# Kernel optimization log

Hardware: AMD Instinct MI355X
Metric: run time of the kernel (lower is better)

Reference implementation:

```python
import jax, jax.numpy as jnp
import numpy as np

EPS = 1e-15
BN_EPS = 1e-5
N_NODES = 50000
N_EDGES = 800000
IN_CH = 32
OUT_CH = 32
DIM = 3


def _gmm_params(key, in_ch, out_ch, K):
    k1, k2, k3, k4 = jax.random.split(key, 4)
    g = jax.random.normal(k1, (in_ch, K * out_ch), jnp.float32) * (1.0 / np.sqrt(in_ch))
    mu = jax.random.normal(k2, (K, DIM), jnp.float32)
    sigma = jax.random.uniform(k3, (K, DIM), jnp.float32, 0.5, 1.5)
    root = jax.random.normal(k4, (in_ch, out_ch), jnp.float32) * (1.0 / np.sqrt(in_ch))
    bias = jnp.zeros((out_ch,), jnp.float32)
    return g, mu, sigma, root, bias


def setup_inputs() -> dict:
    key = jax.random.key(0)
    ks = jax.random.split(key, 12)
    x = jax.random.normal(ks[0], (N_NODES, IN_CH), jnp.float32)
    edge_index = jax.random.randint(ks[1], (2, N_EDGES), 0, N_NODES, jnp.int64)
    edge_attr = jax.random.uniform(ks[2], (N_EDGES, DIM), jnp.float32)
    g1, mu1, sig1, root1, b1 = _gmm_params(ks[3], IN_CH, OUT_CH, 5)
    g2, mu2, sig2, root2, b2 = _gmm_params(ks[4], OUT_CH, OUT_CH, 5)
    gs, mus, sigs, roots, bs = _gmm_params(ks[5], IN_CH, OUT_CH, 1)
    ones = jnp.ones((OUT_CH,), jnp.float32)
    zeros = jnp.zeros((OUT_CH,), jnp.float32)
    return dict(x=x, edge_attr=edge_attr,
                g1=g1, mu1=mu1, sig1=sig1, root1=root1, b1=b1, gam1=ones, bet1=zeros,
                g2=g2, mu2=mu2, sig2=sig2, root2=root2, b2=b2, gam2=ones, bet2=zeros,
                gs=gs, mus=mus, sigs=sigs, roots=roots, bs=bs, gams=ones, bets=zeros,
                edge_index=edge_index)


def gmm_conv(x, edge_index, edge_attr, g, mu, sigma, root, bias, num_nodes):
    # PyG GMMConv (separate kernels=False, aggr='mean', root_weight=True)
    src, dst = edge_index[0], edge_index[1]
    K = mu.shape[0]
    out_ch = root.shape[1]
    # Gaussian mixture weights per edge/kernel: [E, K]
    diff = edge_attr[:, None, :] - mu[None, :, :]               # [E, K, D]
    w = jnp.exp(jnp.sum(-0.5 * diff * diff / (EPS + sigma[None] ** 2), axis=-1))
    # Project and gather source features: [E, K, out]
    xj = (x @ g).reshape(-1, K, out_ch)[src] if False else (x[src] @ g).reshape(-1, K, out_ch)
    msg = jnp.einsum('ek,ekc->ec', w, xj)                        # [E, out]
    agg = jax.ops.segment_sum(msg, dst, num_segments=num_nodes)
    cnt = jax.ops.segment_sum(jnp.ones((msg.shape[0],), msg.dtype), dst, num_segments=num_nodes)
    agg = agg / jnp.maximum(cnt, 1.0)[:, None]                   # mean aggregation
    return agg + x @ root + bias


def batch_norm(x, gamma, beta):
    mean = jnp.mean(x, axis=0)
    var = jnp.var(x, axis=0)
    return gamma * (x - mean) * jax.lax.rsqrt(var + BN_EPS) + beta


def reference(x, edge_attr,
              g1, mu1, sig1, root1, b1, gam1, bet1,
              g2, mu2, sig2, root2, b2, gam2, bet2,
              gs, mus, sigs, roots, bs, gams, bets,
              edge_index):
    n = x.shape[0]
    h = jax.nn.elu(batch_norm(gmm_conv(x, edge_index, edge_attr, g1, mu1, sig1, root1, b1, n), gam1, bet1))
    h = batch_norm(gmm_conv(h, edge_index, edge_attr, g2, mu2, sig2, root2, b2, n), gam2, bet2)
    s = batch_norm(gmm_conv(x, edge_index, edge_attr, gs, mus, sigs, roots, bs, n), gams, bets)
    return jax.nn.elu(h + s)
```

## Files before the change

### kernel.cpp

```cpp
#include <hip/hip_runtime.h>
#include <hip/hip_fp16.h>
#include <math.h>

#define NN 50000
#define NE 800000
#define GEPS 1e-15f
#define BN_EPS 1e-5f
#define NB 196
#define LOG2E 1.4426950408889634f

typedef _Float16 f16x8 __attribute__((ext_vector_type(8)));
typedef float f32x4 __attribute__((ext_vector_type(4)));

__global__ void precompute_gc(const float* __restrict__ sig1, const float* __restrict__ mu1,
                              const float* __restrict__ sig2, const float* __restrict__ mu2,
                              const float* __restrict__ sigs, const float* __restrict__ mus,
                              float* __restrict__ gc) {
    int s = threadIdx.x;
    if (s >= 11) return;
    const float* sg; const float* mu;
    if (s < 5)       { sg = sig1 + s * 3;       mu = mu1 + s * 3; }
    else if (s < 10) { sg = sig2 + (s - 5) * 3; mu = mu2 + (s - 5) * 3; }
    else             { sg = sigs;               mu = mus; }
    float C = 0.f;
    for (int d = 0; d < 3; d++) {
        float sv = sg[d];
        float iv = -0.5f / (GEPS + sv * sv) * LOG2E;
        float m = mu[d];
        gc[s * 8 + d] = iv;
        gc[s * 8 + 3 + d] = -2.f * iv * m;
        C += iv * m * m;
    }
    gc[s * 8 + 6] = C;
    gc[s * 8 + 7] = 0.f;
}

__global__ void hist_kernel(const int* __restrict__ ei, int* __restrict__ deg) {
    int e = blockIdx.x * blockDim.x + threadIdx.x;
    if (e < NE) atomicAdd(&deg[ei[NE + e]], 1);
}

__global__ void block_reduce_kernel(const int* __restrict__ deg, int* __restrict__ bsum) {
    __shared__ int sh[256];
    int t = threadIdx.x;
    int i = blockIdx.x * 256 + t;
    sh[t] = (i < NN) ? deg[i] : 0;
    __syncthreads();
    for (int off = 128; off > 0; off >>= 1) {
        if (t < off) sh[t] += sh[t + off];
        __syncthreads();
    }
    if (t == 0) bsum[blockIdx.x] = sh[0];
}

__global__ void scan_partials_kernel(int* __restrict__ bsum) {
    __shared__ int sh[256];
    int t = threadIdx.x;
    int v = (t < NB) ? bsum[t] : 0;
    sh[t] = v;
    __syncthreads();
    for (int off = 1; off < 256; off <<= 1) {
        int u = (t >= off) ? sh[t - off] : 0;
        __syncthreads();
        sh[t] += u;
        __syncthreads();
    }
    if (t < NB) bsum[t] = sh[t] - v;
}

__global__ void block_scan_kernel(const int* __restrict__ deg, const int* __restrict__ bsum,
                                  int* __restrict__ rowstart, int* __restrict__ cursor) {
    __shared__ int sh[256];
    int t = threadIdx.x;
    int i = blockIdx.x * 256 + t;
    int v = (i < NN) ? deg[i] : 0;
    sh[t] = v;
    __syncthreads();
    for (int off = 1; off < 256; off <<= 1) {
        int u = (t >= off) ? sh[t - off] : 0;
        __syncthreads();
        sh[t] += u;
        __syncthreads();
    }
    int excl = sh[t] - v + bsum[blockIdx.x];
    if (i < NN) { rowstart[i] = excl; cursor[i] = excl; }
}

__global__ void reorder_kernel(const int* __restrict__ ei, const float* __restrict__ ea,
                               int* __restrict__ cursor, int4* __restrict__ rec) {
    int e = blockIdx.x * blockDim.x + threadIdx.x;
    if (e >= NE) return;
    int src = ei[e];
    int dst = ei[NE + e];
    int4 q;
    q.x = src;
    q.y = __float_as_int(ea[e * 3 + 0]);
    q.z = __float_as_int(ea[e * 3 + 1]);
    q.w = __float_as_int(ea[e * 3 + 2]);
    int pos = atomicAdd(&cursor[dst], 1);
    rec[pos] = q;
}

__global__ void projR_kernel(const float* __restrict__ x, const float* __restrict__ root1,
                             const float* __restrict__ b1, const float* __restrict__ roots,
                             const float* __restrict__ bs, __half* __restrict__ xh,
                             float* __restrict__ R1, float* __restrict__ Rs) {
    const int t = threadIdx.x;
    const int col = t & 31;
    const int half_ = (t >> 5) & 1;
    const int rg = t >> 6;
    float w[32];
    const float* rootp = half_ ? roots : root1;
#pragma unroll
    for (int i = 0; i < 32; i++) w[i] = rootp[i * 32 + col];
    float b = half_ ? bs[col] : b1[col];
    float* Rp = half_ ? Rs : R1;
    __shared__ float hs[256];
    for (int n0 = blockIdx.x * 8; n0 < NN; n0 += gridDim.x * 8) {
        float v = x[(size_t)n0 * 32 + t];
        hs[t] = v;
        xh[(size_t)n0 * 32 + t] = __float2half(v);
        __syncthreads();
#pragma unroll
        for (int rr = 0; rr < 2; rr++) {
            int r = rg * 2 + rr;
            float acc = b;
#pragma unroll
            for (int i = 0; i < 32; i++) acc += w[i] * hs[r * 32 + i];
            Rp[(size_t)(n0 + r) * 32 + col] = acc;
        }
        __syncthreads();
    }
}

__global__ void projB2_kernel(const float* __restrict__ c1, const float* __restrict__ stats,
                              const float* __restrict__ gam1, const float* __restrict__ bet1,
                              const float* __restrict__ root2, const float* __restrict__ b2,
                              __half* __restrict__ hh, float* __restrict__ R2) {
    const int t = threadIdx.x;
    const int col = t & 31;
    const int rg = t >> 5;
    __shared__ float sc[32], sf[32];
    if (t < 32) {
        const float invN = 1.0f / (float)NN;
        float m = stats[t] * invN;
        float v = stats[32 + t] * invN - m * m;
        float s = gam1[t] * rsqrtf(v + BN_EPS);
        sc[t] = s;
        sf[t] = bet1[t] - m * s;
    }
    float w[32];
#pragma unroll
    for (int i = 0; i < 32; i++) w[i] = root2[i * 32 + col];
    float b = b2[col];
    __shared__ float hs[256];
    __syncthreads();
    for (int n0 = blockIdx.x * 8; n0 < NN; n0 += gridDim.x * 8) {
        float v = c1[(size_t)n0 * 32 + t];
        float hv = sc[t & 31] * v + sf[t & 31];
        hv = hv > 0.f ? hv : (__expf(hv) - 1.f);
        hs[t] = hv;
        hh[(size_t)n0 * 32 + t] = __float2half(hv);
        __syncthreads();
        float acc = b;
#pragma unroll
        for (int i = 0; i < 32; i++) acc += w[i] * hs[rg * 32 + i];
        R2[(size_t)(n0 + rg) * 32 + col] = acc;
        __syncthreads();
    }
}

template <bool SKIP, int KOFF>
__global__ void agg_kernel(const int4* __restrict__ rec, const int* __restrict__ rowstart,
                           const int* __restrict__ deg, const __half* __restrict__ X,
                           const float* __restrict__ gc, __half* __restrict__ Aout) {
    constexpr int NS = SKIP ? 6 : 5;
    constexpr int SA = SKIP ? 192 : 160;
    const int tid = blockIdx.x * blockDim.x + threadIdx.x;
    const int lane = threadIdx.x & 63;
    const int grp = lane >> 4;
    const int ch2 = lane & 15;
    const int wavesTotal = (gridDim.x * blockDim.x) >> 6;
    const int wid = tid >> 6;

    float cp[NS][3], cq[NS][3], cc[NS];
#pragma unroll
    for (int s = 0; s < NS; s++) {
        int slot = (s < 5) ? (KOFF + s) : 10;
#pragma unroll
        for (int d = 0; d < 3; d++) {
            cp[s][d] = gc[slot * 8 + d];
            cq[s][d] = gc[slot * 8 + 3 + d];
        }
        cc[s] = gc[slot * 8 + 6];
    }

    for (int n = wid; n < NN; n += wavesTotal) {
        const int start = rowstart[n];
        const int d = deg[n];
        float2 acc[NS];
#pragma unroll
        for (int s = 0; s < NS; s++) acc[s] = make_float2(0.f, 0.f);
        for (int i = grp; i < d; i += 4) {
            int4 r = rec[(size_t)(start + i)];
            const __half2 xv = *(const __half2*)(X + (((size_t)r.x) << 5) + 2 * ch2);
            float2 xf = __half22float2(xv);
            float a0 = __int_as_float(r.y), a1 = __int_as_float(r.z), a2 = __int_as_float(r.w);
            float s0 = a0 * a0, s1 = a1 * a1, s2 = a2 * a2;
#pragma unroll
            for (int s = 0; s < NS; s++) {
                float ex = cc[s];
                ex = fmaf(cq[s][0], a0, ex);
                ex = fmaf(cq[s][1], a1, ex);
                ex = fmaf(cq[s][2], a2, ex);
                ex = fmaf(cp[s][0], s0, ex);
                ex = fmaf(cp[s][1], s1, ex);
                ex = fmaf(cp[s][2], s2, ex);
                float w = exp2f(ex);
                acc[s].x = fmaf(w, xf.x, acc[s].x);
                acc[s].y = fmaf(w, xf.y, acc[s].y);
            }
        }
#pragma unroll
        for (int s = 0; s < NS; s++) {
            acc[s].x += __shfl_xor(acc[s].x, 16, 64);
            acc[s].x += __shfl_xor(acc[s].x, 32, 64);
            acc[s].y += __shfl_xor(acc[s].y, 16, 64);
            acc[s].y += __shfl_xor(acc[s].y, 32, 64);
        }
        if (grp == 0) {
            const float invd = 1.0f / fmaxf((float)d, 1.0f);
            __half* base = Aout + (size_t)n * SA + 2 * ch2;
#pragma unroll
            for (int s = 0; s < 5; s++) {
                __half2 hv = __floats2half2_rn(acc[s].x * invd, acc[s].y * invd);
                *(__half2*)(base + s * 32) = hv;
            }
            if (SKIP) {
                __half2 hv = __floats2half2_rn(acc[5].x * invd, acc[5].y * invd);
                *(__half2*)(base + 160) = hv;
            }
        }
    }
}

template <bool SKIP>
__global__ __launch_bounds__(256, 4) void gemm_kernel(
        const __half* __restrict__ Ah, const float* __restrict__ G,
        const float* __restrict__ Gs, const float* __restrict__ R,
        const float* __restrict__ Rs, float* __restrict__ C,
        float* __restrict__ Cs, float* __restrict__ stats) {
    constexpr int SA = SKIP ? 192 : 160;
    const int tid = blockIdx.x * blockDim.x + threadIdx.x;
    const int l = threadIdx.x & 63;
    const int r16 = l & 15;
    const int quad = l >> 4;
    const int wid = tid >> 6;
    const int nw = (gridDim.x * blockDim.x) >> 6;

    f16x8 bf[5][2];
#pragma unroll
    for (int kt = 0; kt < 5; kt++)
#pragma unroll
        for (int ct = 0; ct < 2; ct++)
#pragma unroll
            for (int e = 0; e < 8; e++) {
                int jj = quad * 8 + e;
                bf[kt][ct][e] = (_Float16)G[jj * 160 + kt * 32 + ct * 16 + r16];
            }
    f16x8 bs[2];
    if (SKIP) {
#pragma unroll
        for (int ct = 0; ct < 2; ct++)
#pragma unroll
            for (int e = 0; e < 8; e++) {
                int jj = quad * 8 + e;
                bs[ct][e] = (_Float16)Gs[jj * 32 + ct * 16 + r16];
            }
    }

    float s0 = 0.f, s1 = 0.f, q0 = 0.f, q1 = 0.f;
    float t0 = 0.f, t1 = 0.f, u0 = 0.f, u1 = 0.f;

    for (int tile = wid; tile < NN / 16; tile += nw) {
        const int n0 = tile * 16;
        const __half* arow = Ah + (size_t)(n0 + r16) * SA + quad * 8;
        f32x4 acc0 = {0.f, 0.f, 0.f, 0.f};
        f32x4 acc1 = {0.f, 0.f, 0.f, 0.f};
        f32x4 sa0 = {0.f, 0.f, 0.f, 0.f};
        f32x4 sa1 = {0.f, 0.f, 0.f, 0.f};
#pragma unroll
        for (int kt = 0; kt < 5; kt++) {
            f16x8 a = *(const f16x8*)(arow + kt * 32);
            acc0 = __builtin_amdgcn_mfma_f32_16x16x32_f16(a, bf[kt][0], acc0, 0, 0, 0);
            acc1 = __builtin_amdgcn_mfma_f32_16x16x32_f16(a, bf[kt][1], acc1, 0, 0, 0);
        }
        if (SKIP) {
            f16x8 a = *(const f16x8*)(arow + 160);
            sa0 = __builtin_amdgcn_mfma_f32_16x16x32_f16(a, bs[0], sa0, 0, 0, 0);
            sa1 = __builtin_amdgcn_mfma_f32_16x16x32_f16(a, bs[1], sa1, 0, 0, 0);
        }
#pragma unroll
        for (int r = 0; r < 4; r++) {
            const int nr = n0 + quad * 4 + r;
            const int b = nr * 32;
            {
                float v = acc0[r] + R[b + r16];
                C[b + r16] = v; s0 += v; q0 += v * v;
            }
            {
                float v = acc1[r] + R[b + 16 + r16];
                C[b + 16 + r16] = v; s1 += v; q1 += v * v;
            }
            if (SKIP) {
                float v = sa0[r] + Rs[b + r16];
                Cs[b + r16] = v; t0 += v; u0 += v * v;
                float w2 = sa1[r] + Rs[b + 16 + r16];
                Cs[b + 16 + r16] = w2; t1 += w2; u1 += w2 * w2;
            }
        }
    }
    s0 += __shfl_xor(s0, 16, 64); s0 += __shfl_xor(s0, 32, 64);
    s1 += __shfl_xor(s1, 16, 64); s1 += __shfl_xor(s1, 32, 64);
    q0 += __shfl_xor(q0, 16, 64); q0 += __shfl_xor(q0, 32, 64);
    q1 += __shfl_xor(q1, 16, 64); q1 += __shfl_xor(q1, 32, 64);
    if (SKIP) {
        t0 += __shfl_xor(t0, 16, 64); t0 += __shfl_xor(t0, 32, 64);
        t1 += __shfl_xor(t1, 16, 64); t1 += __shfl_xor(t1, 32, 64);
        u0 += __shfl_xor(u0, 16, 64); u0 += __shfl_xor(u0, 32, 64);
        u1 += __shfl_xor(u1, 16, 64); u1 += __shfl_xor(u1, 32, 64);
    }
    __shared__ float sred[128];
    const int t = threadIdx.x;
    if (t < 128) sred[t] = 0.f;
    __syncthreads();
    if (l < 16) {
        atomicAdd(&sred[l], s0);       atomicAdd(&sred[16 + l], s1);
        atomicAdd(&sred[32 + l], q0);  atomicAdd(&sred[48 + l], q1);
        if (SKIP) {
            atomicAdd(&sred[64 + l], t0);  atomicAdd(&sred[80 + l], t1);
            atomicAdd(&sred[96 + l], u0);  atomicAdd(&sred[112 + l], u1);
        }
    }
    __syncthreads();
    if (SKIP) { if (t < 128) atomicAdd(&stats[t], sred[t]); }
    else      { if (t < 64)  atomicAdd(&stats[t], sred[t]); }
}

__global__ void apply2_kernel(const float* __restrict__ c2, const float* __restrict__ cs,
                              const float* __restrict__ stats, const float* __restrict__ gam2,
                              const float* __restrict__ bet2, const float* __restrict__ gams,
                              const float* __restrict__ bets, float* __restrict__ out) {
    int idx = blockIdx.x * blockDim.x + threadIdx.x;
    if (idx >= NN * 32) return;
    int ch = idx & 31;
    const float invN = 1.0f / (float)NN;
    float m2 = stats[128 + ch] * invN;
    float v2 = stats[160 + ch] * invN - m2 * m2;
    float ms = stats[64 + ch] * invN;
    float vs = stats[96 + ch] * invN - ms * ms;
    float bn2 = gam2[ch] * (c2[idx] - m2) * rsqrtf(v2 + BN_EPS) + bet2[ch];
    float bns = gams[ch] * (cs[idx] - ms) * rsqrtf(vs + BN_EPS) + bets[ch];
    float o = bn2 + bns;
    out[idx] = o > 0.f ? o : (__expf(o) - 1.f);
}

extern "C" void kernel_launch(void* const* d_in, const int* in_sizes, int n_in,
                              void* d_out, int out_size, void* d_ws, size_t ws_size,
                              hipStream_t stream) {
    const float* x     = (const float*)d_in[0];
    const float* ea    = (const float*)d_in[1];
    const float* g1    = (const float*)d_in[2];
    const float* mu1   = (const float*)d_in[3];
    const float* sig1  = (const float*)d_in[4];
    const float* root1 = (const float*)d_in[5];
    const float* b1    = (const float*)d_in[6];
    const float* gam1  = (const float*)d_in[7];
    const float* bet1  = (const float*)d_in[8];
    const float* g2    = (const float*)d_in[9];
    const float* mu2   = (const float*)d_in[10];
    const float* sig2  = (const float*)d_in[11];
    const float* root2 = (const float*)d_in[12];
    const float* b2    = (const float*)d_in[13];
    const float* gam2  = (const float*)d_in[14];
    const float* bet2  = (const float*)d_in[15];
    const float* gs    = (const float*)d_in[16];
    const float* mus   = (const float*)d_in[17];
    const float* sigs  = (const float*)d_in[18];
    const float* roots = (const float*)d_in[19];
    const float* bs    = (const float*)d_in[20];
    const float* gams  = (const float*)d_in[21];
    const float* bets  = (const float*)d_in[22];
    const int*   ei    = (const int*)d_in[23];
    float* out = (float*)d_out;

    char* w = (char*)d_ws;
    __half* xh  = (__half*)w;   w += (size_t)NN * 32 * 2;
    __half* hh  = (__half*)w;   w += (size_t)NN * 32 * 2;
    __half* Ah  = (__half*)w;   w += (size_t)NN * 192 * 2;
    float*  R1  = (float*)w;    w += (size_t)NN * 32 * 4;
    float*  Rs  = (float*)w;    w += (size_t)NN * 32 * 4;
    float*  R2  = (float*)w;    w += (size_t)NN * 32 * 4;
    float*  c1  = (float*)w;    w += (size_t)NN * 32 * 4;
    float*  cs  = (float*)w;    w += (size_t)NN * 32 * 4;
    int4*   rec = (int4*)w;     w += (size_t)NE * 16;
    int*    deg = (int*)w;      w += (size_t)NN * 4;
    int*    rowstart = (int*)w; w += (size_t)NN * 4;
    int*    cursor   = (int*)w; w += (size_t)NN * 4;
    int*    bsum = (int*)w;     w += 256 * 4;
    float*  stats = (float*)w;  w += 256 * 4;
    float*  gc    = (float*)w;  w += 11 * 8 * 4;

    const int edgeBlocks  = (NE + 255) / 256;
    const int applyBlocks = (NN * 32 + 255) / 256;

    hipMemsetAsync(deg, 0, NN * sizeof(int), stream);
    hipMemsetAsync(stats, 0, 256 * sizeof(float), stream);
    precompute_gc<<<1, 16, 0, stream>>>(sig1, mu1, sig2, mu2, sigs, mus, gc);

    hist_kernel<<<edgeBlocks, 256, 0, stream>>>(ei, deg);
    block_reduce_kernel<<<NB, 256, 0, stream>>>(deg, bsum);
    scan_partials_kernel<<<1, 256, 0, stream>>>(bsum);
    block_scan_kernel<<<NB, 256, 0, stream>>>(deg, bsum, rowstart, cursor);
    reorder_kernel<<<edgeBlocks, 256, 0, stream>>>(ei, ea, cursor, rec);

    projR_kernel<<<1024, 256, 0, stream>>>(x, root1, b1, roots, bs, xh, R1, Rs);
    agg_kernel<true, 0><<<2048, 256, 0, stream>>>(rec, rowstart, deg, xh, gc, Ah);
    gemm_kernel<true><<<512, 256, 0, stream>>>(Ah, g1, gs, R1, Rs, c1, cs, stats);

    projB2_kernel<<<1024, 256, 0, stream>>>(c1, stats, gam1, bet1, root2, b2, hh, R2);
    agg_kernel<false, 5><<<2048, 256, 0, stream>>>(rec, rowstart, deg, hh, gc, Ah);
    gemm_kernel<false><<<512, 256, 0, stream>>>(Ah, g2, nullptr, R2, nullptr, c1, nullptr,
                                                stats + 128);
    apply2_kernel<<<applyBlocks, 256, 0, stream>>>(c1, cs, stats, gam2, bet2, gams, bets, out);
}
```

Before: 361.8 us.

## Precompute Gaussian edge weights in reorder pass as fp16 records

```diff
diff --git a/kernel.cpp b/kernel.cpp
--- a/kernel.cpp
+++ b/kernel.cpp
@@ -11,6 +11,11 @@
 
 typedef _Float16 f16x8 __attribute__((ext_vector_type(8)));
 typedef float f32x4 __attribute__((ext_vector_type(4)));
+
+__device__ __forceinline__ float2 h2f(unsigned int u) {
+    __half2 h = *reinterpret_cast<const __half2*>(&u);
+    return __half22float2(h);
+}
 
 __global__ void precompute_gc(const float* __restrict__ sig1, const float* __restrict__ mu1,
                               const float* __restrict__ sig2, const float* __restrict__ mu2,
@@ -87,18 +92,40 @@
 }
 
 __global__ void reorder_kernel(const int* __restrict__ ei, const float* __restrict__ ea,
-                               int* __restrict__ cursor, int4* __restrict__ rec) {
+                               const float* __restrict__ gc, int* __restrict__ cursor,
+                               int4* __restrict__ recA, int4* __restrict__ recB) {
     int e = blockIdx.x * blockDim.x + threadIdx.x;
     if (e >= NE) return;
     int src = ei[e];
     int dst = ei[NE + e];
-    int4 q;
-    q.x = src;
-    q.y = __float_as_int(ea[e * 3 + 0]);
-    q.z = __float_as_int(ea[e * 3 + 1]);
-    q.w = __float_as_int(ea[e * 3 + 2]);
+    float a0 = ea[e * 3 + 0], a1 = ea[e * 3 + 1], a2 = ea[e * 3 + 2];
+    float s0 = a0 * a0, s1 = a1 * a1, s2 = a2 * a2;
+
+    __half wv[11];
+#pragma unroll
+    for (int s = 0; s < 11; s++) {
+        float ex = gc[s * 8 + 6];
+        ex = fmaf(gc[s * 8 + 3], a0, ex);
+        ex = fmaf(gc[s * 8 + 4], a1, ex);
+        ex = fmaf(gc[s * 8 + 5], a2, ex);
+        ex = fmaf(gc[s * 8 + 0], s0, ex);
+        ex = fmaf(gc[s * 8 + 1], s1, ex);
+        ex = fmaf(gc[s * 8 + 2], s2, ex);
+        wv[s] = __float2half(exp2f(ex));
+    }
+
+    union UA { struct { int src; __half w[6]; } r; int4 q; } ua;
+    ua.r.src = src;
+    ua.r.w[0] = wv[0]; ua.r.w[1] = wv[1]; ua.r.w[2] = wv[2];
+    ua.r.w[3] = wv[3]; ua.r.w[4] = wv[4]; ua.r.w[5] = wv[10];
+    union UB { struct { int src; __half w[5]; __half pad; } r; int4 q; } ub;
+    ub.r.src = src;
+    ub.r.w[0] = wv[5]; ub.r.w[1] = wv[6]; ub.r.w[2] = wv[7];
+    ub.r.w[3] = wv[8]; ub.r.w[4] = wv[9]; ub.r.pad = __float2half(0.f);
+
     int pos = atomicAdd(&cursor[dst], 1);
-    rec[pos] = q;
+    recA[pos] = ua.q;
+    recB[pos] = ub.q;
 }
 
 __global__ void projR_kernel(const float* __restrict__ x, const float* __restrict__ root1,
@@ -170,10 +197,10 @@
     }
 }
 
-template <bool SKIP, int KOFF>
+template <bool SKIP>
 __global__ void agg_kernel(const int4* __restrict__ rec, const int* __restrict__ rowstart,
                            const int* __restrict__ deg, const __half* __restrict__ X,
-                           const float* __restrict__ gc, __half* __restrict__ Aout) {
+                           __half* __restrict__ Aout) {
     constexpr int NS = SKIP ? 6 : 5;
     constexpr int SA = SKIP ? 192 : 160;
     const int tid = blockIdx.x * blockDim.x + threadIdx.x;
@@ -183,18 +210,6 @@
     const int wavesTotal = (gridDim.x * blockDim.x) >> 6;
     const int wid = tid >> 6;
 
-    float cp[NS][3], cq[NS][3], cc[NS];
-#pragma unroll
-    for (int s = 0; s < NS; s++) {
-        int slot = (s < 5) ? (KOFF + s) : 10;
-#pragma unroll
-        for (int d = 0; d < 3; d++) {
-            cp[s][d] = gc[slot * 8 + d];
-            cq[s][d] = gc[slot * 8 + 3 + d];
-        }
-        cc[s] = gc[slot * 8 + 6];
-    }
-
     for (int n = wid; n < NN; n += wavesTotal) {
         const int start = rowstart[n];
         const int d = deg[n];
@@ -205,20 +220,14 @@
             int4 r = rec[(size_t)(start + i)];
             const __half2 xv = *(const __half2*)(X + (((size_t)r.x) << 5) + 2 * ch2);
             float2 xf = __half22float2(xv);
-            float a0 = __int_as_float(r.y), a1 = __int_as_float(r.z), a2 = __int_as_float(r.w);
-            float s0 = a0 * a0, s1 = a1 * a1, s2 = a2 * a2;
+            float2 w01 = h2f((unsigned)r.y);
+            float2 w23 = h2f((unsigned)r.z);
+            float2 w45 = h2f((unsigned)r.w);
+            float wv[6] = {w01.x, w01.y, w23.x, w23.y, w45.x, w45.y};
 #pragma unroll
             for (int s = 0; s < NS; s++) {
-                float ex = cc[s];
-                ex = fmaf(cq[s][0], a0, ex);
-                ex = fmaf(cq[s][1], a1, ex);
-                ex = fmaf(cq[s][2], a2, ex);
-                ex = fmaf(cp[s][0], s0, ex);
-                ex = fmaf(cp[s][1], s1, ex);
-                ex = fmaf(cp[s][2], s2, ex);
-                float w = exp2f(ex);
-                acc[s].x = fmaf(w, xf.x, acc[s].x);
-                acc[s].y = fmaf(w, xf.y, acc[s].y);
+                acc[s].x = fmaf(wv[s], xf.x, acc[s].x);
+                acc[s].y = fmaf(wv[s], xf.y, acc[s].y);
             }
         }
 #pragma unroll
@@ -403,7 +412,8 @@
     float*  R2  = (float*)w;    w += (size_t)NN * 32 * 4;
     float*  c1  = (float*)w;    w += (size_t)NN * 32 * 4;
     float*  cs  = (float*)w;    w += (size_t)NN * 32 * 4;
-    int4*   rec = (int4*)w;     w += (size_t)NE * 16;
+    int4*   recA = (int4*)w;    w += (size_t)NE * 16;
+    int4*   recB = (int4*)w;    w += (size_t)NE * 16;
     int*    deg = (int*)w;      w += (size_t)NN * 4;
     int*    rowstart = (int*)w; w += (size_t)NN * 4;
     int*    cursor   = (int*)w; w += (size_t)NN * 4;
@@ -422,14 +432,14 @@
     block_reduce_kernel<<<NB, 256, 0, stream>>>(deg, bsum);
     scan_partials_kernel<<<1, 256, 0, stream>>>(bsum);
     block_scan_kernel<<<NB, 256, 0, stream>>>(deg, bsum, rowstart, cursor);
-    reorder_kernel<<<edgeBlocks, 256, 0, stream>>>(ei, ea, cursor, rec);
+    reorder_kernel<<<edgeBlocks, 256, 0, stream>>>(ei, ea, gc, cursor, recA, recB);
 
     projR_kernel<<<1024, 256, 0, stream>>>(x, root1, b1, roots, bs, xh, R1, Rs);
-    agg_kernel<true, 0><<<2048, 256, 0, stream>>>(rec, rowstart, deg, xh, gc, Ah);
+    agg_kernel<true><<<2048, 256, 0, stream>>>(recA, rowstart, deg, xh, Ah);
     gemm_kernel<true><<<512, 256, 0, stream>>>(Ah, g1, gs, R1, Rs, c1, cs, stats);
 
     projB2_kernel<<<1024, 256, 0, stream>>>(c1, stats, gam1, bet1, root2, b2, hh, R2);
-    agg_kernel<false, 5><<<2048, 256, 0, stream>>>(rec, rowstart, deg, hh, gc, Ah);
+    agg_kernel<false><<<2048, 256, 0, stream>>>(recB, rowstart, deg, hh, Ah);
     gemm_kernel<false><<<512, 256, 0, stream>>>(Ah, g2, nullptr, R2, nullptr, c1, nullptr,
                                                 stats + 128);
     apply2_kernel<<<applyBlocks, 256, 0, stream>>>(c1, cs, stats, gam2, bet2, gams, bets, out);
```

New measurement: 328.2 us. -9.3%, faster.
